# Kernel optimization log

Hardware: AMD Instinct MI355X
Metric: run time of the kernel (lower is better)

Reference implementation:

```python
import jax, jax.numpy as jnp
import numpy as np

TEMPERATURE = 0.07
N_CLASSES = 100


def setup_inputs() -> dict:
    key = jax.random.key(0)
    k1, k2 = jax.random.split(key)
    N, D = 8192, 128
    emb = jax.random.normal(k1, (N, D), dtype=jnp.float32)
    # unit-normalize so exp(sim / temperature) stays finite in fp32
    emb = emb / jnp.linalg.norm(emb, axis=1, keepdims=True)
    labels = jax.random.randint(k2, (N,), 0, N_CLASSES, dtype=jnp.int64)
    return {"embeddings": emb, "labels": labels}


def reference(embeddings, labels):
    N = embeddings.shape[0]
    dt = embeddings.dtype
    # [N, N] similarity
    sim = jnp.matmul(embeddings, embeddings.T) / TEMPERATURE
    off_diag = 1.0 - jnp.eye(N, dtype=dt)
    pos_mask = (labels[:, None] == labels[None, :]).astype(dt) * off_diag
    exp_sim = jnp.exp(sim) * off_diag  # diagonal zeroed
    positive_sum = jnp.sum(exp_sim * pos_mask, axis=1)
    total_sum = jnp.sum(exp_sim, axis=1)
    loss = -jnp.log(positive_sum / (total_sum + 1e-8) + 1e-8)
    valid = pos_mask.sum(axis=1) > 0
    cnt = jnp.sum(valid.astype(dt))
    mean_loss = jnp.where(
        cnt > 0,
        jnp.sum(jnp.where(valid, loss, jnp.zeros_like(loss))) / jnp.maximum(cnt, 1.0),
        jnp.asarray(0.0, dtype=dt),
    )
    return mean_loss
```

## Files before the change

kernel.cpp:

```cpp
#include <hip/hip_runtime.h>

#define N 8192
#define D 128
#define SCALE_A 20.6098592f
#define NBX 64
#define NBY 8
#define NBLK (NBX * NBY)

using short8  = __attribute__((ext_vector_type(8))) short;
using float4v = __attribute__((ext_vector_type(4))) float;

#if __has_builtin(__builtin_amdgcn_exp2f)
#define EXP2(x) __builtin_amdgcn_exp2f(x)
#else
#define EXP2(x) __expf((x) * 0.69314718f)
#endif

static __device__ inline unsigned int f2bf(float f) {
    union { float f; unsigned int u; } x;
    x.f = f;
    unsigned int u = x.u;
    return (u + 0x7FFFu + ((u >> 16) & 1u)) >> 16;
}

__global__ __launch_bounds__(256) void cl_prep(
    const float* __restrict__ emb, unsigned short* __restrict__ bfB,
    unsigned short* __restrict__ bfA, float* __restrict__ tot,
    int* __restrict__ ticket)
{
    const int t = blockIdx.x * 256 + threadIdx.x;
    const float* p = emb + (size_t)t * 16;
    uint4 ob[2], oa[2];
    #pragma unroll
    for (int h = 0; h < 2; ++h) {
        float4v f0 = *(const float4v*)(p + h * 8);
        float4v f1 = *(const float4v*)(p + h * 8 + 4);
        ob[h].x = f2bf(f0[0]) | (f2bf(f0[1]) << 16);
        ob[h].y = f2bf(f0[2]) | (f2bf(f0[3]) << 16);
        ob[h].z = f2bf(f1[0]) | (f2bf(f1[1]) << 16);
        ob[h].w = f2bf(f1[2]) | (f2bf(f1[3]) << 16);
        oa[h].x = f2bf(f0[0] * SCALE_A) | (f2bf(f0[1] * SCALE_A) << 16);
        oa[h].y = f2bf(f0[2] * SCALE_A) | (f2bf(f0[3] * SCALE_A) << 16);
        oa[h].z = f2bf(f1[0] * SCALE_A) | (f2bf(f1[1] * SCALE_A) << 16);
        oa[h].w = f2bf(f1[2] * SCALE_A) | (f2bf(f1[3] * SCALE_A) << 16);
    }
    ((uint4*)bfB)[t * 2]     = ob[0];
    ((uint4*)bfB)[t * 2 + 1] = ob[1];
    ((uint4*)bfA)[t * 2]     = oa[0];
    ((uint4*)bfA)[t * 2 + 1] = oa[1];
    if (t < 2 * N) tot[t] = 0.f;
    if (t == 0) *ticket = 0;
}

static __device__ __forceinline__ void stage_tile(
    const uint4* __restrict__ bfB4, int cbase, uint4* lds_dst, int tid)
{
    const uint4* src = bfB4 + (size_t)cbase * 16;
    #pragma unroll
    for (int i = 0; i < 8; ++i) {
        const int g     = tid + i * 256;
        const int row   = g >> 4;
        const int chunk = g & 15;
        __builtin_amdgcn_global_load_lds(
            (const __attribute__((address_space(1))) void*)(src + row * 16 + (chunk ^ (row & 15))),
            (__attribute__((address_space(3))) void*)(lds_dst + g),
            16, 0, 0);
    }
}

__global__ __launch_bounds__(256, 2) void cl_main(
    const unsigned short* __restrict__ bfA, const unsigned short* __restrict__ bfB,
    const int* __restrict__ labels,
    float* __restrict__ tot, float* __restrict__ pos,
    int* __restrict__ ticket, float* __restrict__ out)
{
    __shared__ uint4 ldsB[2][128 * 16];
    __shared__ int   s_collab[1024];
    __shared__ float sred[2][4];
    __shared__ int   s_ticket;

    const int tid  = threadIdx.x;
    const int lane = tid & 63;
    const int wave = tid >> 6;
    const int q    = lane >> 4;
    const int c    = lane & 15;
    const int rw     = blockIdx.x * 128 + wave * 32;
    const int cbase0 = blockIdx.y * 1024;
    const uint4* bfB4 = (const uint4*)bfB;

    stage_tile(bfB4, cbase0, &ldsB[0][0], tid);

    short8 afrag[2][4];
    int rowlab[2][4];
    #pragma unroll
    for (int tr = 0; tr < 2; ++tr) {
        const int arow = rw + tr * 16 + c;
        #pragma unroll
        for (int ks = 0; ks < 4; ++ks)
            afrag[tr][ks] = *(const short8*)(bfA + (size_t)arow * D + ks * 32 + q * 8);
        #pragma unroll
        for (int reg = 0; reg < 4; ++reg)
            rowlab[tr][reg] = labels[rw + tr * 16 + q * 4 + reg];
    }

    {
        int4 lv = *(const int4*)(labels + cbase0 + tid * 4);
        *(int4*)(&s_collab[tid * 4]) = lv;
    }
    asm volatile("s_waitcnt lgkmcnt(0)" ::: "memory");
    __builtin_amdgcn_s_barrier();

    float tot_a[2][4] = {{0.f,0.f,0.f,0.f},{0.f,0.f,0.f,0.f}};
    float pos_a[2][4] = {{0.f,0.f,0.f,0.f},{0.f,0.f,0.f,0.f}};

    int cur = 0;
    #pragma unroll 1
    for (int it = 0; it < 8; ++it) {
        if (it < 7) {
            stage_tile(bfB4, cbase0 + (it + 1) * 128, &ldsB[cur ^ 1][0], tid);
            asm volatile("s_waitcnt vmcnt(8)" ::: "memory");
        } else {
            asm volatile("s_waitcnt vmcnt(0)" ::: "memory");
        }
        __builtin_amdgcn_s_barrier();
        __builtin_amdgcn_sched_barrier(0);

        int collab[8];
        #pragma unroll
        for (int tc = 0; tc < 8; ++tc) collab[tc] = s_collab[it * 128 + tc * 16 + c];

        float4v acc[2][8];
        #pragma unroll
        for (int tr = 0; tr < 2; ++tr)
            #pragma unroll
            for (int tc = 0; tc < 8; ++tc) {
                float4v z = {0.f, 0.f, 0.f, 0.f};
                acc[tr][tc] = z;
            }

        const short8* ldsS = (const short8*)&ldsB[cur][0];
        #pragma unroll
        for (int ks = 0; ks < 4; ++ks) {
            const short8* pk = ldsS + c * 16 + ((ks * 4 + q) ^ c);
            #pragma unroll
            for (int tc = 0; tc < 8; ++tc) {
                short8 b = pk[tc * 256];
                #pragma unroll
                for (int tr = 0; tr < 2; ++tr)
                    acc[tr][tc] = __builtin_amdgcn_mfma_f32_16x16x32_bf16(
                        afrag[tr][ks], b, acc[tr][tc], 0, 0, 0);
            }
        }

        const int cbase = cbase0 + it * 128;
        #pragma unroll
        for (int tr = 0; tr < 2; ++tr) {
            const int rtile = rw + tr * 16;
            #pragma unroll
            for (int tc = 0; tc < 8; ++tc) {
                const bool diag_tile = (rtile == cbase + tc * 16);
                const int lc = collab[tc];
                #pragma unroll
                for (int reg = 0; reg < 4; ++reg) {
                    float v = EXP2(acc[tr][tc][reg]);
                    if (diag_tile && (q * 4 + reg) == c) v = 0.f;
                    tot_a[tr][reg] += v;
                    if (rowlab[tr][reg] == lc) pos_a[tr][reg] += v;
                }
            }
        }

        __builtin_amdgcn_sched_barrier(0);
        __builtin_amdgcn_s_barrier();
        cur ^= 1;
    }

    #pragma unroll
    for (int tr = 0; tr < 2; ++tr)
        #pragma unroll
        for (int reg = 0; reg < 4; ++reg) {
            float t = tot_a[tr][reg];
            float p = pos_a[tr][reg];
            #pragma unroll
            for (int m = 1; m < 16; m <<= 1) {
                t += __shfl_xor(t, m, 64);
                p += __shfl_xor(p, m, 64);
            }
            if (c == 0) {
                const int r = rw + tr * 16 + q * 4 + reg;
                atomicAdd(&tot[r], t);
                atomicAdd(&pos[r], p);
            }
        }

    asm volatile("s_waitcnt vmcnt(0)" ::: "memory");
    __syncthreads();
    if (tid == 0)
        s_ticket = __hip_atomic_fetch_add(ticket, 1, __ATOMIC_RELAXED,
                                          __HIP_MEMORY_SCOPE_AGENT);
    __syncthreads();
    if (s_ticket != NBLK - 1) return;

    float lsum = 0.f, lcnt = 0.f;
    #pragma unroll 4
    for (int i = tid; i < N; i += 256) {
        const float t = __hip_atomic_load(&tot[i], __ATOMIC_RELAXED,
                                          __HIP_MEMORY_SCOPE_AGENT);
        const float p = __hip_atomic_load(&pos[i], __ATOMIC_RELAXED,
                                          __HIP_MEMORY_SCOPE_AGENT);
        const float loss = -__logf(p / (t + 1e-8f) + 1e-8f);
        if (p > 0.f) { lsum += loss; lcnt += 1.f; }
    }
    #pragma unroll
    for (int m = 1; m < 64; m <<= 1) {
        lsum += __shfl_xor(lsum, m, 64);
        lcnt += __shfl_xor(lcnt, m, 64);
    }
    if (lane == 0) { sred[0][wave] = lsum; sred[1][wave] = lcnt; }
    __syncthreads();
    if (tid == 0) {
        const float s = sred[0][0] + sred[0][1] + sred[0][2] + sred[0][3];
        const float n = sred[1][0] + sred[1][1] + sred[1][2] + sred[1][3];
        out[0] = (n > 0.f) ? s / fmaxf(n, 1.f) : 0.f;
    }
}

extern "C" void kernel_launch(void* const* d_in, const int* in_sizes, int n_in,
                              void* d_out, int out_size, void* d_ws, size_t ws_size,
                              hipStream_t stream) {
    const float* emb  = (const float*)d_in[0];
    const int* labels = (const int*)d_in[1];
    unsigned short* bfB = (unsigned short*)d_ws;
    unsigned short* bfA = bfB + (size_t)N * D;
    float* tot    = (float*)(bfA + (size_t)N * D);
    float* pos    = tot + N;
    int*   ticket = (int*)(pos + N);

    cl_prep<<<256, 256, 0, stream>>>(emb, bfB, bfA, tot, ticket);
    cl_main<<<dim3(NBX, NBY), 256, 0, stream>>>(bfA, bfB, labels, tot, pos,
                                                ticket, (float*)d_out);
}
```

Before: 93.37 us.

## Fuse bf16 conversion into main kernel and replace atomics with flagged partials

After: 150.6 us. +61.3%, slower.

```diff
diff --git a/kernel.cpp b/kernel.cpp
--- a/kernel.cpp
+++ b/kernel.cpp
@@ -6,6 +6,7 @@
 #define NBX 64
 #define NBY 8
 #define NBLK (NBX * NBY)
+#define FLAG_MAGIC 0x5CA1AB1Eu
 
 using short8  = __attribute__((ext_vector_type(8))) short;
 using float4v = __attribute__((ext_vector_type(4))) float;
@@ -23,61 +24,41 @@
     return (u + 0x7FFFu + ((u >> 16) & 1u)) >> 16;
 }
 
-__global__ __launch_bounds__(256) void cl_prep(
-    const float* __restrict__ emb, unsigned short* __restrict__ bfB,
-    unsigned short* __restrict__ bfA, float* __restrict__ tot,
-    int* __restrict__ ticket)
+static __device__ __forceinline__ void issue_tile(
+    const float4v* __restrict__ emb4, int cbase, int trow, int tc8,
+    float4v (&r)[16])
 {
-    const int t = blockIdx.x * 256 + threadIdx.x;
-    const float* p = emb + (size_t)t * 16;
-    uint4 ob[2], oa[2];
-    #pragma unroll
-    for (int h = 0; h < 2; ++h) {
-        float4v f0 = *(const float4v*)(p + h * 8);
-        float4v f1 = *(const float4v*)(p + h * 8 + 4);
-        ob[h].x = f2bf(f0[0]) | (f2bf(f0[1]) << 16);
-        ob[h].y = f2bf(f0[2]) | (f2bf(f0[3]) << 16);
-        ob[h].z = f2bf(f1[0]) | (f2bf(f1[1]) << 16);
-        ob[h].w = f2bf(f1[2]) | (f2bf(f1[3]) << 16);
-        oa[h].x = f2bf(f0[0] * SCALE_A) | (f2bf(f0[1] * SCALE_A) << 16);
-        oa[h].y = f2bf(f0[2] * SCALE_A) | (f2bf(f0[3] * SCALE_A) << 16);
-        oa[h].z = f2bf(f1[0] * SCALE_A) | (f2bf(f1[1] * SCALE_A) << 16);
-        oa[h].w = f2bf(f1[2] * SCALE_A) | (f2bf(f1[3] * SCALE_A) << 16);
-    }
-    ((uint4*)bfB)[t * 2]     = ob[0];
-    ((uint4*)bfB)[t * 2 + 1] = ob[1];
-    ((uint4*)bfA)[t * 2]     = oa[0];
-    ((uint4*)bfA)[t * 2 + 1] = oa[1];
-    if (t < 2 * N) tot[t] = 0.f;
-    if (t == 0) *ticket = 0;
-}
-
-static __device__ __forceinline__ void stage_tile(
-    const uint4* __restrict__ bfB4, int cbase, uint4* lds_dst, int tid)
+    #pragma unroll
+    for (int ch = 0; ch < 8; ++ch) {
+        const size_t o = (size_t)(cbase + trow + ch * 16) * 32 + tc8 * 2;
+        r[2 * ch]     = emb4[o];
+        r[2 * ch + 1] = emb4[o + 1];
+    }
+}
+
+static __device__ __forceinline__ void convert_write(
+    const float4v (&r)[16], uint4* dst)
 {
-    const uint4* src = bfB4 + (size_t)cbase * 16;
-    #pragma unroll
-    for (int i = 0; i < 8; ++i) {
-        const int g     = tid + i * 256;
-        const int row   = g >> 4;
-        const int chunk = g & 15;
-        __builtin_amdgcn_global_load_lds(
-            (const __attribute__((address_space(1))) void*)(src + row * 16 + (chunk ^ (row & 15))),
-            (__attribute__((address_space(3))) void*)(lds_dst + g),
-            16, 0, 0);
-    }
-}
-
-__global__ __launch_bounds__(256, 2) void cl_main(
-    const unsigned short* __restrict__ bfA, const unsigned short* __restrict__ bfB,
-    const int* __restrict__ labels,
-    float* __restrict__ tot, float* __restrict__ pos,
-    int* __restrict__ ticket, float* __restrict__ out)
+    #pragma unroll
+    for (int ch = 0; ch < 8; ++ch) {
+        const float4v f0 = r[2 * ch], f1 = r[2 * ch + 1];
+        uint4 w;
+        w.x = f2bf(f0[0]) | (f2bf(f0[1]) << 16);
+        w.y = f2bf(f0[2]) | (f2bf(f0[3]) << 16);
+        w.z = f2bf(f1[0]) | (f2bf(f1[1]) << 16);
+        w.w = f2bf(f1[2]) | (f2bf(f1[3]) << 16);
+        dst[ch * 256] = w;
+    }
+}
+
+__global__ __launch_bounds__(256, 2) void cl_fused(
+    const float* __restrict__ emb, const int* __restrict__ labels,
+    float* __restrict__ part, unsigned int* __restrict__ flags,
+    float* __restrict__ out)
 {
-    __shared__ uint4 ldsB[2][128 * 16];
+    __shared__ uint4 ldsB[128 * 16];
     __shared__ int   s_collab[1024];
     __shared__ float sred[2][4];
-    __shared__ int   s_ticket;
 
     const int tid  = threadIdx.x;
     const int lane = tid & 63;
@@ -86,9 +67,13 @@
     const int c    = lane & 15;
     const int rw     = blockIdx.x * 128 + wave * 32;
     const int cbase0 = blockIdx.y * 1024;
-    const uint4* bfB4 = (const uint4*)bfB;
-
-    stage_tile(bfB4, cbase0, &ldsB[0][0], tid);
+    const int bid    = blockIdx.y * NBX + blockIdx.x;
+    const int trow   = tid >> 4;
+    const int tc8    = tid & 15;
+    const float4v* emb4 = (const float4v*)emb;
+
+    float4v r[16];
+    issue_tile(emb4, cbase0, trow, tc8, r);
 
     short8 afrag[2][4];
     int rowlab[2][4];
@@ -96,8 +81,16 @@
     for (int tr = 0; tr < 2; ++tr) {
         const int arow = rw + tr * 16 + c;
         #pragma unroll
-        for (int ks = 0; ks < 4; ++ks)
-            afrag[tr][ks] = *(const short8*)(bfA + (size_t)arow * D + ks * 32 + q * 8);
+        for (int ks = 0; ks < 4; ++ks) {
+            const float4v a0 = emb4[(size_t)arow * 32 + ks * 8 + q * 2];
+            const float4v a1 = emb4[(size_t)arow * 32 + ks * 8 + q * 2 + 1];
+            union { short8 s; uint4 u; } w;
+            w.u.x = f2bf(a0[0] * SCALE_A) | (f2bf(a0[1] * SCALE_A) << 16);
+            w.u.y = f2bf(a0[2] * SCALE_A) | (f2bf(a0[3] * SCALE_A) << 16);
+            w.u.z = f2bf(a1[0] * SCALE_A) | (f2bf(a1[1] * SCALE_A) << 16);
+            w.u.w = f2bf(a1[2] * SCALE_A) | (f2bf(a1[3] * SCALE_A) << 16);
+            afrag[tr][ks] = w.s;
+        }
         #pragma unroll
         for (int reg = 0; reg < 4; ++reg)
             rowlab[tr][reg] = labels[rw + tr * 16 + q * 4 + reg];
@@ -107,24 +100,19 @@
         int4 lv = *(const int4*)(labels + cbase0 + tid * 4);
         *(int4*)(&s_collab[tid * 4]) = lv;
     }
+
+    uint4* dst = &ldsB[trow * 16 + (tc8 ^ trow)];
+    convert_write(r, dst);
+    issue_tile(emb4, cbase0 + 128, trow, tc8, r);
     asm volatile("s_waitcnt lgkmcnt(0)" ::: "memory");
     __builtin_amdgcn_s_barrier();
+    __builtin_amdgcn_sched_barrier(0);
 
     float tot_a[2][4] = {{0.f,0.f,0.f,0.f},{0.f,0.f,0.f,0.f}};
     float pos_a[2][4] = {{0.f,0.f,0.f,0.f},{0.f,0.f,0.f,0.f}};
 
-    int cur = 0;
     #pragma unroll 1
     for (int it = 0; it < 8; ++it) {
-        if (it < 7) {
-            stage_tile(bfB4, cbase0 + (it + 1) * 128, &ldsB[cur ^ 1][0], tid);
-            asm volatile("s_waitcnt vmcnt(8)" ::: "memory");
-        } else {
-            asm volatile("s_waitcnt vmcnt(0)" ::: "memory");
-        }
-        __builtin_amdgcn_s_barrier();
-        __builtin_amdgcn_sched_barrier(0);
-
         int collab[8];
         #pragma unroll
         for (int tc = 0; tc < 8; ++tc) collab[tc] = s_collab[it * 128 + tc * 16 + c];
@@ -138,7 +126,7 @@
                 acc[tr][tc] = z;
             }
 
-        const short8* ldsS = (const short8*)&ldsB[cur][0];
+        const short8* ldsS = (const short8*)ldsB;
         #pragma unroll
         for (int ks = 0; ks < 4; ++ks) {
             const short8* pk = ldsS + c * 16 + ((ks * 4 + q) ^ c);
@@ -172,7 +160,15 @@
 
         __builtin_amdgcn_sched_barrier(0);
         __builtin_amdgcn_s_barrier();
-        cur ^= 1;
+        __builtin_amdgcn_sched_barrier(0);
+
+        if (it < 7) {
+            convert_write(r, dst);
+            if (it < 6) issue_tile(emb4, cbase0 + (it + 2) * 128, trow, tc8, r);
+            asm volatile("s_waitcnt lgkmcnt(0)" ::: "memory");
+            __builtin_amdgcn_s_barrier();
+            __builtin_amdgcn_sched_barrier(0);
+        }
     }
 
     #pragma unroll
@@ -187,29 +183,39 @@
                 p += __shfl_xor(p, m, 64);
             }
             if (c == 0) {
-                const int r = rw + tr * 16 + q * 4 + reg;
-                atomicAdd(&tot[r], t);
-                atomicAdd(&pos[r], p);
+                const int rrow = rw + tr * 16 + q * 4 + reg;
+                __hip_atomic_store(&part[rrow * 16 + blockIdx.y], t,
+                                   __ATOMIC_RELAXED, __HIP_MEMORY_SCOPE_AGENT);
+                __hip_atomic_store(&part[rrow * 16 + 8 + blockIdx.y], p,
+                                   __ATOMIC_RELAXED, __HIP_MEMORY_SCOPE_AGENT);
             }
         }
 
     asm volatile("s_waitcnt vmcnt(0)" ::: "memory");
     __syncthreads();
     if (tid == 0)
-        s_ticket = __hip_atomic_fetch_add(ticket, 1, __ATOMIC_RELAXED,
-                                          __HIP_MEMORY_SCOPE_AGENT);
+        __hip_atomic_store(&flags[bid], FLAG_MAGIC, __ATOMIC_RELAXED,
+                           __HIP_MEMORY_SCOPE_AGENT);
+    if (bid != 0) return;
+
+    while (__hip_atomic_load(&flags[tid], __ATOMIC_RELAXED,
+                             __HIP_MEMORY_SCOPE_AGENT) != FLAG_MAGIC) {}
+    while (__hip_atomic_load(&flags[tid + 256], __ATOMIC_RELAXED,
+                             __HIP_MEMORY_SCOPE_AGENT) != FLAG_MAGIC) {}
     __syncthreads();
-    if (s_ticket != NBLK - 1) return;
 
     float lsum = 0.f, lcnt = 0.f;
-    #pragma unroll 4
-    for (int i = tid; i < N; i += 256) {
-        const float t = __hip_atomic_load(&tot[i], __ATOMIC_RELAXED,
-                                          __HIP_MEMORY_SCOPE_AGENT);
-        const float p = __hip_atomic_load(&pos[i], __ATOMIC_RELAXED,
-                                          __HIP_MEMORY_SCOPE_AGENT);
-        const float loss = -__logf(p / (t + 1e-8f) + 1e-8f);
-        if (p > 0.f) { lsum += loss; lcnt += 1.f; }
+    for (int rrow = tid; rrow < N; rrow += 256) {
+        float ts = 0.f, ps = 0.f;
+        #pragma unroll
+        for (int y = 0; y < NBY; ++y) {
+            ts += __hip_atomic_load(&part[rrow * 16 + y], __ATOMIC_RELAXED,
+                                    __HIP_MEMORY_SCOPE_AGENT);
+            ps += __hip_atomic_load(&part[rrow * 16 + 8 + y], __ATOMIC_RELAXED,
+                                    __HIP_MEMORY_SCOPE_AGENT);
+        }
+        const float loss = -__logf(ps / (ts + 1e-8f) + 1e-8f);
+        if (ps > 0.f) { lsum += loss; lcnt += 1.f; }
     }
     #pragma unroll
     for (int m = 1; m < 64; m <<= 1) {
@@ -230,13 +236,9 @@
                               hipStream_t stream) {
     const float* emb  = (const float*)d_in[0];
     const int* labels = (const int*)d_in[1];
-    unsigned short* bfB = (unsigned short*)d_ws;
-    unsigned short* bfA = bfB + (size_t)N * D;
-    float* tot    = (float*)(bfA + (size_t)N * D);
-    float* pos    = tot + N;
-    int*   ticket = (int*)(pos + N);
-
-    cl_prep<<<256, 256, 0, stream>>>(emb, bfB, bfA, tot, ticket);
-    cl_main<<<dim3(NBX, NBY), 256, 0, stream>>>(bfA, bfB, labels, tot, pos,
-                                                ticket, (float*)d_out);
-}
+    float* part = (float*)d_ws;
+    unsigned int* flags = (unsigned int*)(part + (size_t)N * 16);
+
+    cl_fused<<<dim3(NBX, NBY), 256, 0, stream>>>(emb, labels, part, flags,
+                                                 (float*)d_out);
+}
```

## Single-buffer LDS, split accumulators into two passes, double grid for occupancy

Applied to the files above, without the earlier changes.

Result: slower. 130.3 us (+39.6%).

```diff
diff --git a/kernel.cpp b/kernel.cpp
--- a/kernel.cpp
+++ b/kernel.cpp
@@ -4,8 +4,9 @@
 #define D 128
 #define SCALE_A 20.6098592f
 #define NBX 64
-#define NBY 8
+#define NBY 16
 #define NBLK (NBX * NBY)
+#define ITERS 4
 
 using short8  = __attribute__((ext_vector_type(8))) short;
 using float4v = __attribute__((ext_vector_type(4))) float;
@@ -68,14 +69,14 @@
     }
 }
 
-__global__ __launch_bounds__(256, 2) void cl_main(
+__global__ __launch_bounds__(256, 4) void cl_main(
     const unsigned short* __restrict__ bfA, const unsigned short* __restrict__ bfB,
     const int* __restrict__ labels,
     float* __restrict__ tot, float* __restrict__ pos,
     int* __restrict__ ticket, float* __restrict__ out)
 {
-    __shared__ uint4 ldsB[2][128 * 16];
-    __shared__ int   s_collab[1024];
+    __shared__ uint4 ldsB[128 * 16];
+    __shared__ int   s_collab[512];
     __shared__ float sred[2][4];
     __shared__ int   s_ticket;
 
@@ -85,10 +86,10 @@
     const int q    = lane >> 4;
     const int c    = lane & 15;
     const int rw     = blockIdx.x * 128 + wave * 32;
-    const int cbase0 = blockIdx.y * 1024;
+    const int cbase0 = blockIdx.y * 512;
     const uint4* bfB4 = (const uint4*)bfB;
 
-    stage_tile(bfB4, cbase0, &ldsB[0][0], tid);
+    stage_tile(bfB4, cbase0, &ldsB[0], tid);
 
     short8 afrag[2][4];
     int rowlab[2][4];
@@ -104,75 +105,79 @@
     }
 
     {
-        int4 lv = *(const int4*)(labels + cbase0 + tid * 4);
-        *(int4*)(&s_collab[tid * 4]) = lv;
-    }
-    asm volatile("s_waitcnt lgkmcnt(0)" ::: "memory");
+        int2 lv = *(const int2*)(labels + cbase0 + tid * 2);
+        *(int2*)(&s_collab[tid * 2]) = lv;
+    }
+    asm volatile("s_waitcnt vmcnt(0) lgkmcnt(0)" ::: "memory");
     __builtin_amdgcn_s_barrier();
+    __builtin_amdgcn_sched_barrier(0);
 
     float tot_a[2][4] = {{0.f,0.f,0.f,0.f},{0.f,0.f,0.f,0.f}};
     float pos_a[2][4] = {{0.f,0.f,0.f,0.f},{0.f,0.f,0.f,0.f}};
 
-    int cur = 0;
     #pragma unroll 1
-    for (int it = 0; it < 8; ++it) {
-        if (it < 7) {
-            stage_tile(bfB4, cbase0 + (it + 1) * 128, &ldsB[cur ^ 1][0], tid);
-            asm volatile("s_waitcnt vmcnt(8)" ::: "memory");
-        } else {
-            asm volatile("s_waitcnt vmcnt(0)" ::: "memory");
+    for (int it = 0; it < ITERS; ++it) {
+        const int cbase = cbase0 + it * 128;
+        int collab[8];
+        #pragma unroll
+        for (int tc = 0; tc < 8; ++tc) collab[tc] = s_collab[it * 128 + tc * 16 + c];
+
+        const short8* ldsS = (const short8*)ldsB;
+
+        #pragma unroll
+        for (int pass = 0; pass < 2; ++pass) {
+            float4v acc[2][4];
+            #pragma unroll
+            for (int tr = 0; tr < 2; ++tr)
+                #pragma unroll
+                for (int tcl = 0; tcl < 4; ++tcl) {
+                    float4v z = {0.f, 0.f, 0.f, 0.f};
+                    acc[tr][tcl] = z;
+                }
+
+            #pragma unroll
+            for (int ks = 0; ks < 4; ++ks) {
+                const short8* pk = ldsS + c * 16 + ((ks * 4 + q) ^ c);
+                #pragma unroll
+                for (int tcl = 0; tcl < 4; ++tcl) {
+                    const int tc = pass * 4 + tcl;
+                    short8 b = pk[tc * 256];
+                    #pragma unroll
+                    for (int tr = 0; tr < 2; ++tr)
+                        acc[tr][tcl] = __builtin_amdgcn_mfma_f32_16x16x32_bf16(
+                            afrag[tr][ks], b, acc[tr][tcl], 0, 0, 0);
+                }
+            }
+
+            #pragma unroll
+            for (int tr = 0; tr < 2; ++tr) {
+                const int rtile = rw + tr * 16;
+                #pragma unroll
+                for (int tcl = 0; tcl < 4; ++tcl) {
+                    const int tc = pass * 4 + tcl;
+                    const bool diag_tile = (rtile == cbase + tc * 16);
+                    const int lc = collab[tc];
+                    #pragma unroll
+                    for (int reg = 0; reg < 4; ++reg) {
+                        float v = EXP2(acc[tr][tcl][reg]);
+                        if (diag_tile && (q * 4 + reg) == c) v = 0.f;
+                        tot_a[tr][reg] += v;
+                        if (rowlab[tr][reg] == lc) pos_a[tr][reg] += v;
+                    }
+                }
+            }
         }
+
+        __builtin_amdgcn_sched_barrier(0);
         __builtin_amdgcn_s_barrier();
         __builtin_amdgcn_sched_barrier(0);
 
-        int collab[8];
-        #pragma unroll
-        for (int tc = 0; tc < 8; ++tc) collab[tc] = s_collab[it * 128 + tc * 16 + c];
-
-        float4v acc[2][8];
-        #pragma unroll
-        for (int tr = 0; tr < 2; ++tr)
-            #pragma unroll
-            for (int tc = 0; tc < 8; ++tc) {
-                float4v z = {0.f, 0.f, 0.f, 0.f};
-                acc[tr][tc] = z;
-            }
-
-        const short8* ldsS = (const short8*)&ldsB[cur][0];
-        #pragma unroll
-        for (int ks = 0; ks < 4; ++ks) {
-            const short8* pk = ldsS + c * 16 + ((ks * 4 + q) ^ c);
-            #pragma unroll
-            for (int tc = 0; tc < 8; ++tc) {
-                short8 b = pk[tc * 256];
-                #pragma unroll
-                for (int tr = 0; tr < 2; ++tr)
-                    acc[tr][tc] = __builtin_amdgcn_mfma_f32_16x16x32_bf16(
-                        afrag[tr][ks], b, acc[tr][tc], 0, 0, 0);
-            }
+        if (it < ITERS - 1) {
+            stage_tile(bfB4, cbase0 + (it + 1) * 128, &ldsB[0], tid);
+            asm volatile("s_waitcnt vmcnt(0)" ::: "memory");
+            __builtin_amdgcn_s_barrier();
+            __builtin_amdgcn_sched_barrier(0);
         }
-
-        const int cbase = cbase0 + it * 128;
-        #pragma unroll
-        for (int tr = 0; tr < 2; ++tr) {
-            const int rtile = rw + tr * 16;
-            #pragma unroll
-            for (int tc = 0; tc < 8; ++tc) {
-                const bool diag_tile = (rtile == cbase + tc * 16);
-                const int lc = collab[tc];
-                #pragma unroll
-                for (int reg = 0; reg < 4; ++reg) {
-                    float v = EXP2(acc[tr][tc][reg]);
-                    if (diag_tile && (q * 4 + reg) == c) v = 0.f;
-                    tot_a[tr][reg] += v;
-                    if (rowlab[tr][reg] == lc) pos_a[tr][reg] += v;
-                }
-            }
-        }
-
-        __builtin_amdgcn_sched_barrier(0);
-        __builtin_amdgcn_s_barrier();
-        cur ^= 1;
     }
 
     #pragma unroll
```
